# Kernel tuning notes

Measured on AMD Instinct MI355X. Metric: run time of the kernel, lower is better.

The kernel has to match this reference:

```python
import jax, jax.numpy as jnp
import numpy as np

D_MODEL = 1024
NHEADS = 16
DIM_K = D_MODEL // NHEADS


def setup_inputs() -> dict:
    key = jax.random.key(0)
    ks = jax.random.split(key, 7)
    B, S = 4, 2048
    scale = 1.0 / np.sqrt(D_MODEL)
    return {
        "Q": jax.random.normal(ks[0], (B, S, D_MODEL), jnp.float32),
        "K": jax.random.normal(ks[1], (B, S, D_MODEL), jnp.float32),
        "V": jax.random.normal(ks[2], (B, S, D_MODEL), jnp.float32),
        "Wq": jax.random.normal(ks[3], (D_MODEL, D_MODEL), jnp.float32) * scale,
        "Wk": jax.random.normal(ks[4], (D_MODEL, D_MODEL), jnp.float32) * scale,
        "Wv": jax.random.normal(ks[5], (D_MODEL, D_MODEL), jnp.float32) * scale,
        "Wo": jax.random.normal(ks[6], (D_MODEL, D_MODEL), jnp.float32) * scale,
    }


def _split(x):
    # [B,S,D] -> [B,H,S,dk]
    B, S, _ = x.shape
    return x.reshape(B, S, NHEADS, DIM_K).transpose(0, 2, 1, 3)


def reference(Q, K, V, Wq, Wk, Wv, Wo):
    # nn.Linear(x) = x @ W.T; weights stored torch-style [out, in]
    q = _split(Q @ Wq.T)  # [B,H,S,dk]
    k = _split(K @ Wk.T)
    v = _split(V @ Wv.T)
    scores = jnp.einsum("bhsd,bhtd->bhst", q, k) / jnp.sqrt(jnp.float32(DIM_K))
    attn = jax.nn.softmax(scores, axis=-1)
    out = jnp.einsum("bhst,bhtd->bhsd", attn, v)  # [B,H,S,dk]
    B, H, S, dk = out.shape
    out = out.transpose(0, 2, 1, 3).reshape(B, S, H * dk)
    return out @ Wo.T
```

## Files before the change

### kernel.cpp

```cpp
#include <hip/hip_runtime.h>
#include <math.h>
#include <stdint.h>

#define D_MODEL 1024
#define NHEADS  16
#define DK      64
#define BATCH   4
#define SEQ     2048
#define MROWS   (BATCH * SEQ)
#define TENS    ((size_t)MROWS * D_MODEL)
#define WELT    ((size_t)D_MODEL * D_MODEL)

typedef __attribute__((ext_vector_type(8))) _Float16 f16x8;
typedef __attribute__((ext_vector_type(2))) __fp16 h16x2;
typedef __attribute__((ext_vector_type(4))) float f32x4;
typedef __attribute__((ext_vector_type(8))) unsigned short us8;
typedef __attribute__((ext_vector_type(4))) unsigned short us4;

__device__ __forceinline__ unsigned short f2h(float x) {
    _Float16 h = (_Float16)x;
    return __builtin_bit_cast(unsigned short, h);
}

#if __has_builtin(__builtin_amdgcn_exp2f)
__device__ __forceinline__ float fexp2(float x) { return __builtin_amdgcn_exp2f(x); }
#else
__device__ __forceinline__ float fexp2(float x) { return exp2f(x); }
#endif

__device__ __forceinline__ void gld_lds16(const void* g, void* l) {
    __builtin_amdgcn_global_load_lds(
        (__attribute__((address_space(1))) void*)(uintptr_t)(g),
        (__attribute__((address_space(3))) void*)(unsigned)(uintptr_t)(l),
        16, 0, 0);
}

__global__ __launch_bounds__(256)
void convert_kernel(const float* __restrict__ q, const float* __restrict__ k,
                    const float* __restrict__ v, const float* __restrict__ wq,
                    const float* __restrict__ wk, const float* __restrict__ wv,
                    const float* __restrict__ wo, unsigned short* __restrict__ dst)
{
    const int seg = blockIdx.y;
    size_t i = ((size_t)blockIdx.x * 256 + threadIdx.x) * 4;
    const float* src;
    size_t doff, soff;
    if (seg < 3) {
        if (i >= TENS) return;
        src = (seg == 0) ? q : (seg == 1) ? k : v;
        soff = i;
        doff = (size_t)seg * TENS + i;
    } else {
        if (i >= 4 * WELT) return;
        const int widx = (int)(i >> 20);
        src = (widx == 0) ? wq : (widx == 1) ? wk : (widx == 2) ? wv : wo;
        soff = i & (WELT - 1);
        doff = 3 * TENS + i;
    }
    float4 f = *(const float4*)(src + soff);
    us4 o = { f2h(f.x), f2h(f.y), f2h(f.z), f2h(f.w) };
    *(us4*)(dst + doff) = o;
}

__device__ __forceinline__
void gemm_body8(const unsigned short* __restrict__ A,
                const unsigned short* __restrict__ B,
                void* __restrict__ C, int N, int K, int omode,
                int bm, int bn,
                unsigned short* As, unsigned short* Bs)
{
    const int tid  = threadIdx.x;
    const int wave = tid >> 6;
    const int lane = tid & 63;
    const int g    = lane >> 4;
    const int m15  = lane & 15;

    const int srw = lane >> 3;
    const int lc  = (lane & 7) ^ srw;

    const int wr = (wave >> 1) * 64;
    const int wc = (wave & 1) * 64;

    f32x4 acc[4][4];
#pragma unroll
    for (int i = 0; i < 4; ++i)
#pragma unroll
        for (int j = 0; j < 4; ++j) acc[i][j] = (f32x4){0.f, 0.f, 0.f, 0.f};

    auto stage = [&](int buf, int t) {
        const int k0 = t * 64;
#pragma unroll
        for (int i = 0; i < 4; ++i) {
            const int rb = i * 64 + wave * 8;
            gld_lds16(A + (size_t)(bm + rb + srw) * K + k0 + lc * 8,
                      &As[buf * (256 * 64) + rb * 64]);
        }
#pragma unroll
        for (int j = 0; j < 2; ++j) {
            const int rb = j * 64 + wave * 8;
            gld_lds16(B + (size_t)(bn + rb + srw) * K + k0 + lc * 8,
                      &Bs[buf * (128 * 64) + rb * 64]);
        }
    };

    auto compute = [&](int buf) {
        const unsigned short* Ab = &As[buf * (256 * 64)];
        const unsigned short* Bb = &Bs[buf * (128 * 64)];
#pragma unroll
        for (int t = 0; t < 2; ++t) {
            f16x8 af[4], bf[4];
#pragma unroll
            for (int i = 0; i < 4; ++i) {
                int row = wr + i * 16 + m15;
                int pc  = (4 * t + g) ^ (row & 7);
                af[i] = *(const f16x8*)&Ab[row * 64 + pc * 8];
            }
#pragma unroll
            for (int j = 0; j < 4; ++j) {
                int row = wc + j * 16 + m15;
                int pc  = (4 * t + g) ^ (row & 7);
                bf[j] = *(const f16x8*)&Bb[row * 64 + pc * 8];
            }
            __builtin_amdgcn_s_setprio(1);
#pragma unroll
            for (int i = 0; i < 4; ++i)
#pragma unroll
                for (int j = 0; j < 4; ++j)
                    acc[i][j] = __builtin_amdgcn_mfma_f32_16x16x32_f16(
                        af[i], bf[j], acc[i][j], 0, 0, 0);
            __builtin_amdgcn_s_setprio(0);
        }
    };

    const int NT = K / 64;
    stage(0, 0);
    stage(1, 1);
    int cur = 0;
    for (int t = 0; t < NT; ++t) {
        if (t + 2 < NT) {
            int nb = cur + 2; if (nb >= 3) nb -= 3;
            stage(nb, t + 2);
            asm volatile("s_waitcnt vmcnt(12)" ::: "memory");
        } else if (t + 1 < NT) {
            asm volatile("s_waitcnt vmcnt(6)" ::: "memory");
        } else {
            asm volatile("s_waitcnt vmcnt(0)" ::: "memory");
        }
        __builtin_amdgcn_s_barrier();
        __builtin_amdgcn_sched_barrier(0);
        compute(cur);
        __builtin_amdgcn_sched_barrier(0);
        __builtin_amdgcn_s_barrier();
        ++cur; if (cur == 3) cur = 0;
    }

#pragma unroll
    for (int i = 0; i < 4; ++i) {
        const int gm0 = bm + wr + i * 16 + g * 4;
#pragma unroll
        for (int j = 0; j < 4; ++j) {
            const int gn = bn + wc + j * 16 + m15;
            if (omode == 0) {
#pragma unroll
                for (int r = 0; r < 4; ++r)
                    ((float*)C)[(size_t)(gm0 + r) * N + gn] = acc[i][j][r];
            } else if (omode == 1) {
#pragma unroll
                for (int r = 0; r < 4; ++r)
                    ((unsigned short*)C)[(size_t)(gm0 + r) * N + gn] = f2h(acc[i][j][r]);
            } else {
                const int b_ = gm0 >> 11, s_ = gm0 & 2047;
                const int h_ = gn >> 6,  d_ = gn & 63;
                us4 o = { f2h(acc[i][j][0]), f2h(acc[i][j][1]),
                          f2h(acc[i][j][2]), f2h(acc[i][j][3]) };
                *(us4*)((unsigned short*)C +
                        (((size_t)(b_ * NHEADS + h_) * 256 + (s_ >> 3)) * 64 + d_) * 8
                        + (s_ & 7)) = o;
            }
        }
    }
}

__device__ __forceinline__ void panel_decode(int f, int& bm, int& bn) {
    const int x = f & 7;
    const int k = f >> 3;
    const int panel = x * 4 + (k >> 3);
    const int ny = k & 7;
    bm = panel * 256;
    bn = ny * 128;
}

__global__ __launch_bounds__(512)
void proj3_kernel(const unsigned short* __restrict__ qb,
                  const unsigned short* __restrict__ kb,
                  const unsigned short* __restrict__ vb,
                  const unsigned short* __restrict__ wq,
                  const unsigned short* __restrict__ wk,
                  const unsigned short* __restrict__ wv,
                  unsigned short* __restrict__ qproj,
                  unsigned short* __restrict__ kproj,
                  unsigned short* __restrict__ vtw)
{
    __shared__ unsigned short As[3 * 256 * 64];
    __shared__ unsigned short Bs[3 * 128 * 64];
    const int z = blockIdx.z;
    const unsigned short* A = (z == 0) ? qb : (z == 1) ? kb : vb;
    const unsigned short* B = (z == 0) ? wq : (z == 1) ? wk : wv;
    void* C = (z == 0) ? (void*)qproj : (z == 1) ? (void*)kproj : (void*)vtw;
    int bm, bn;
    panel_decode(blockIdx.x, bm, bn);
    gemm_body8(A, B, C, D_MODEL, D_MODEL, (z == 2) ? 2 : 1, bm, bn, As, Bs);
}

__global__ __launch_bounds__(512)
void gemm_out_kernel(const unsigned short* __restrict__ A,
                     const unsigned short* __restrict__ B,
                     float* __restrict__ C)
{
    __shared__ unsigned short As[3 * 256 * 64];
    __shared__ unsigned short Bs[3 * 128 * 64];
    int bm, bn;
    panel_decode(blockIdx.x, bm, bn);
    gemm_body8(A, B, C, D_MODEL, D_MODEL, 0, bm, bn, As, Bs);
}

__global__ __launch_bounds__(256, 2)
void attn_kernel(const unsigned short* __restrict__ qp,
                 const unsigned short* __restrict__ kp,
                 const unsigned short* __restrict__ vt,
                 unsigned short* __restrict__ ao)
{
    __shared__ unsigned short Ks[2][64 * 64];
    __shared__ unsigned short VTs[2][64 * 64];
    __shared__ unsigned short Ps[4][16 * 64];

    const int tid = threadIdx.x;
    const int w = tid >> 6, lane = tid & 63;
    const int g = lane >> 4, m15 = lane & 15;

    const int f = blockIdx.x;
    const int bh = (f & 7) * 8 + ((f >> 3) >> 3);
    const int qt = (f >> 3) & 7;
    const int b = bh >> 4, h = bh & 15;

    const int q0 = qt * 256 + w * 64;
    const size_t rowbase = (size_t)b * SEQ;

    const int srw = lane >> 3;
    const int lc  = (lane & 7) ^ srw;

    const _Float16 qscale = (_Float16)(0.125f * 1.4426950408889634f);
    f16x8 qf[4][2];
#pragma unroll
    for (int mi = 0; mi < 4; ++mi)
#pragma unroll
        for (int t = 0; t < 2; ++t) {
            f16x8 v = *(const f16x8*)(qp + (rowbase + q0 + mi * 16 + m15) * D_MODEL
                                      + h * DK + t * 32 + g * 8);
            qf[mi][t] = v * qscale;
        }

    const _Float16 one16 = (_Float16)1.f;
    const f16x8 onesf = { one16, one16, one16, one16, one16, one16, one16, one16 };

    float mrun[4] = {-INFINITY, -INFINITY, -INFINITY, -INFINITY};
    float lrun[4] = {0.f, 0.f, 0.f, 0.f};

    f32x4 accO[4][4];
#pragma unroll
    for (int mi = 0; mi < 4; ++mi)
#pragma unroll
        for (int i = 0; i < 4; ++i) accO[mi][i] = (f32x4){0.f, 0.f, 0.f, 0.f};

    const unsigned short* kbase = kp + rowbase * D_MODEL + h * DK;
    const unsigned short* vbase = vt + (size_t)(b * NHEADS + h) * DK * SEQ;

    auto stage = [&](int buf, int t) {
#pragma unroll
        for (int it = 0; it < 2; ++it) {
            const int rb = w * 16 + it * 8;
            gld_lds16(kbase + (size_t)(t * 64 + rb + srw) * D_MODEL + lc * 8,
                      &Ks[buf][rb * 64]);
            gld_lds16(vbase + ((size_t)(t * 8 + lc) * 64 + rb + srw) * 8,
                      &VTs[buf][rb * 64]);
        }
    };

    const int NT = SEQ / 64;
    stage(0, 0);
    __syncthreads();

    for (int kt = 0; kt < NT; ++kt) {
        const int cur = kt & 1;
        if (kt + 1 < NT) stage(cur ^ 1, kt + 1);

        f32x4 ST[4][4];
        __builtin_amdgcn_s_setprio(1);
#pragma unroll
        for (int km = 0; km < 4; ++km) {
            const int row = km * 16 + m15;
            f16x8 kf0 = *(const f16x8*)&Ks[cur][row * 64 + ((0 + g) ^ (row & 7)) * 8];
            f16x8 kf1 = *(const f16x8*)&Ks[cur][row * 64 + ((4 + g) ^ (row & 7)) * 8];
#pragma unroll
            for (int mi = 0; mi < 4; ++mi) {
                f32x4 z = (f32x4){0.f, 0.f, 0.f, 0.f};
                z = __builtin_amdgcn_mfma_f32_16x16x32_f16(kf0, qf[mi][0], z, 0, 0, 0);
                z = __builtin_amdgcn_mfma_f32_16x16x32_f16(kf1, qf[mi][1], z, 0, 0, 0);
                ST[km][mi] = z;
            }
        }
        __builtin_amdgcn_s_setprio(0);

        float lmx[4];
#pragma unroll
        for (int mi = 0; mi < 4; ++mi) {
            float t0 = fmaxf(fmaxf(ST[0][mi][0], ST[0][mi][1]), ST[0][mi][2]);
            float t1 = fmaxf(fmaxf(ST[0][mi][3], ST[1][mi][0]), ST[1][mi][1]);
            float t2 = fmaxf(fmaxf(ST[1][mi][2], ST[1][mi][3]), ST[2][mi][0]);
            float t3 = fmaxf(fmaxf(ST[2][mi][1], ST[2][mi][2]), ST[2][mi][3]);
            float t4 = fmaxf(fmaxf(ST[3][mi][0], ST[3][mi][1]), ST[3][mi][2]);
            float u0 = fmaxf(fmaxf(t0, t1), t2);
            float u1 = fmaxf(fmaxf(t3, t4), ST[3][mi][3]);
            lmx[mi] = fmaxf(u0, u1);
        }

        const float THR = 8.f;
        int need = (lmx[0] > mrun[0] + THR) | (lmx[1] > mrun[1] + THR) |
                   (lmx[2] > mrun[2] + THR) | (lmx[3] > mrun[3] + THR);
        if (__any(need)) {
#pragma unroll
            for (int mi = 0; mi < 4; ++mi) {
                float mx = fmaxf(lmx[mi], __shfl_xor(lmx[mi], 16));
                mx = fmaxf(mx, __shfl_xor(mx, 32));
                float mnew = fmaxf(mrun[mi], mx);
                float scl = fexp2(mrun[mi] - mnew);
                mrun[mi] = mnew;
                lrun[mi] *= scl;
#pragma unroll
                for (int i = 0; i < 4; ++i) accO[mi][i] *= scl;
            }
        }

        f16x8 pf[4][2];
#pragma unroll
        for (int mi = 0; mi < 4; ++mi) {
            const float mnew = mrun[mi];
#pragma unroll
            for (int km = 0; km < 4; ++km) {
                float p0 = fexp2(ST[km][mi][0] - mnew);
                float p1 = fexp2(ST[km][mi][1] - mnew);
                float p2 = fexp2(ST[km][mi][2] - mnew);
                float p3 = fexp2(ST[km][mi][3] - mnew);
                h16x2 d0 = __builtin_amdgcn_cvt_pkrtz(p0, p1);
                h16x2 d1 = __builtin_amdgcn_cvt_pkrtz(p2, p3);
                uint2 wv = { __builtin_bit_cast(unsigned, d0),
                             __builtin_bit_cast(unsigned, d1) };
                const int pc = (km * 2 + (g >> 1)) ^ (m15 & 7);
                *(uint2*)&Ps[w][m15 * 64 + pc * 8 + (g & 1) * 4] = wv;
            }
            pf[mi][0] = *(const f16x8*)&Ps[w][m15 * 64 + ((0 + g) ^ (m15 & 7)) * 8];
            pf[mi][1] = *(const f16x8*)&Ps[w][m15 * 64 + ((4 + g) ^ (m15 & 7)) * 8];
            f32x4 zs = (f32x4){0.f, 0.f, 0.f, 0.f};
            zs = __builtin_amdgcn_mfma_f32_16x16x32_f16(onesf, pf[mi][0], zs, 0, 0, 0);
            zs = __builtin_amdgcn_mfma_f32_16x16x32_f16(onesf, pf[mi][1], zs, 0, 0, 0);
            lrun[mi] += zs[0];
        }

        __builtin_amdgcn_s_setprio(1);
#pragma unroll
        for (int i = 0; i < 4; ++i) {
            const int row = i * 16 + m15;
            f16x8 vf0 = *(const f16x8*)&VTs[cur][row * 64 + ((0 + g) ^ (row & 7)) * 8];
            f16x8 vf1 = *(const f16x8*)&VTs[cur][row * 64 + ((4 + g) ^ (row & 7)) * 8];
#pragma unroll
            for (int mi = 0; mi < 4; ++mi) {
                f32x4 a = accO[mi][i];
                a = __builtin_amdgcn_mfma_f32_16x16x32_f16(vf0, pf[mi][0], a, 0, 0, 0);
                a = __builtin_amdgcn_mfma_f32_16x16x32_f16(vf1, pf[mi][1], a, 0, 0, 0);
                accO[mi][i] = a;
            }
        }
        __builtin_amdgcn_s_setprio(0);

        __syncthreads();
    }

#pragma unroll
    for (int mi = 0; mi < 4; ++mi) {
        const float li = 1.f / lrun[mi];
        const size_t qg = rowbase + q0 + mi * 16 + m15;
#pragma unroll
        for (int i = 0; i < 4; ++i) {
            us4 o = { f2h(accO[mi][i][0] * li), f2h(accO[mi][i][1] * li),
                      f2h(accO[mi][i][2] * li), f2h(accO[mi][i][3] * li) };
            *(us4*)(ao + qg * D_MODEL + h * DK + i * 16 + g * 4) = o;
        }
    }
}

extern "C" void kernel_launch(void* const* d_in, const int* in_sizes, int n_in,
                              void* d_out, int out_size, void* d_ws, size_t ws_size,
                              hipStream_t stream)
{
    const float* Q  = (const float*)d_in[0];
    const float* K  = (const float*)d_in[1];
    const float* V  = (const float*)d_in[2];
    const float* Wq = (const float*)d_in[3];
    const float* Wk = (const float*)d_in[4];
    const float* Wv = (const float*)d_in[5];
    const float* Wo = (const float*)d_in[6];

    unsigned short* base = (unsigned short*)d_ws;
    unsigned short* qb = base;
    unsigned short* kb = qb + TENS;
    unsigned short* vb = kb + TENS;
    unsigned short* wq = vb + TENS;
    unsigned short* wk = wq + WELT;
    unsigned short* wv = wk + WELT;
    unsigned short* wo = wv + WELT;
    unsigned short* qproj = wo + WELT;
    unsigned short* kproj = qproj + TENS;
    unsigned short* vtw   = kproj + TENS;
    unsigned short* aow   = vtw + TENS;

    convert_kernel<<<dim3(TENS / 1024, 4), 256, 0, stream>>>(Q, K, V, Wq, Wk, Wv, Wo, base);

    proj3_kernel<<<dim3(256, 1, 3), 512, 0, stream>>>(
        qb, kb, vb, wq, wk, wv, qproj, kproj, vtw);

    attn_kernel<<<dim3(512, 1, 1), 256, 0, stream>>>(
        qproj, kproj, vtw, aow);

    gemm_out_kernel<<<dim3(256, 1, 1), 512, 0, stream>>>(
        aow, wo, (float*)d_out);
}
```

Measured before the change: 320.6 us.

## Fuse fp32-to-fp16 activation conversion into projection GEMM loads

The separate convert pass over Q, K and V is removed. The projection GEMM now loads fp32 activations into registers, converts them to fp16 and writes them to LDS itself, using a new double-buffered pipeline with two blocks per CU. This drops a full read/write round trip of three 32 MB tensors plus their fp16 copies. In exchange the GEMM reads twice as many bytes for A and carries more register pressure. Separately, the attention kernel now writes all four P tiles to shared memory before reading any back, which enlarges Ps to 32 KB.

```diff
diff --git a/kernel.cpp b/kernel.cpp
--- a/kernel.cpp
+++ b/kernel.cpp
@@ -36,36 +36,194 @@
 }
 
 __global__ __launch_bounds__(256)
-void convert_kernel(const float* __restrict__ q, const float* __restrict__ k,
-                    const float* __restrict__ v, const float* __restrict__ wq,
-                    const float* __restrict__ wk, const float* __restrict__ wv,
-                    const float* __restrict__ wo, unsigned short* __restrict__ dst)
-{
-    const int seg = blockIdx.y;
+void convert_w_kernel(const float* __restrict__ wq, const float* __restrict__ wk,
+                      const float* __restrict__ wv, const float* __restrict__ wo,
+                      unsigned short* __restrict__ dst)
+{
     size_t i = ((size_t)blockIdx.x * 256 + threadIdx.x) * 4;
-    const float* src;
-    size_t doff, soff;
-    if (seg < 3) {
-        if (i >= TENS) return;
-        src = (seg == 0) ? q : (seg == 1) ? k : v;
-        soff = i;
-        doff = (size_t)seg * TENS + i;
-    } else {
-        if (i >= 4 * WELT) return;
-        const int widx = (int)(i >> 20);
-        src = (widx == 0) ? wq : (widx == 1) ? wk : (widx == 2) ? wv : wo;
-        soff = i & (WELT - 1);
-        doff = 3 * TENS + i;
-    }
+    const int widx = (int)(i >> 20);
+    const float* src = (widx == 0) ? wq : (widx == 1) ? wk : (widx == 2) ? wv : wo;
+    const size_t soff = i & (WELT - 1);
     float4 f = *(const float4*)(src + soff);
     us4 o = { f2h(f.x), f2h(f.y), f2h(f.z), f2h(f.w) };
-    *(us4*)(dst + doff) = o;
+    *(us4*)(dst + i) = o;
+}
+
+__device__ __forceinline__ void panel_decode(int f, int& bm, int& bn) {
+    const int x = f & 7;
+    const int k = f >> 3;
+    const int panel = x * 4 + (k >> 3);
+    const int ny = k & 7;
+    bm = panel * 256;
+    bn = ny * 128;
+}
+
+__device__ __forceinline__
+void gemm_body_cvt(const float* __restrict__ A32,
+                   const unsigned short* __restrict__ Bh,
+                   void* __restrict__ C, int N, int K, int omode,
+                   int bm, int bn,
+                   unsigned short* As, unsigned short* Bs)
+{
+    const int tid  = threadIdx.x;
+    const int wave = tid >> 6;
+    const int lane = tid & 63;
+    const int g    = lane >> 4;
+    const int m15  = lane & 15;
+
+    const int srw = lane >> 3;
+    const int lc  = (lane & 7) ^ srw;
+
+    const int wr = (wave >> 1) * 64;
+    const int wc = (wave & 1) * 64;
+
+    const int arow = tid >> 1;
+    const int ac0  = (tid & 1) * 4;
+
+    f32x4 acc[4][4];
+#pragma unroll
+    for (int i = 0; i < 4; ++i)
+#pragma unroll
+        for (int j = 0; j < 4; ++j) acc[i][j] = (f32x4){0.f, 0.f, 0.f, 0.f};
+
+    auto loadA = [&](float4* r, int t) {
+        const float* s = A32 + (size_t)(bm + arow) * K + t * 64 + ac0 * 8;
+#pragma unroll
+        for (int c = 0; c < 4; ++c) {
+            r[2 * c]     = *(const float4*)(s + c * 8);
+            r[2 * c + 1] = *(const float4*)(s + c * 8 + 4);
+        }
+    };
+    auto writeA = [&](int buf, const float4* r) {
+#pragma unroll
+        for (int c = 0; c < 4; ++c) {
+            us8 o = { f2h(r[2*c].x),   f2h(r[2*c].y),   f2h(r[2*c].z),   f2h(r[2*c].w),
+                      f2h(r[2*c+1].x), f2h(r[2*c+1].y), f2h(r[2*c+1].z), f2h(r[2*c+1].w) };
+            const int pc = (ac0 + c) ^ (arow & 7);
+            *(us8*)&As[buf * (256 * 64) + arow * 64 + pc * 8] = o;
+        }
+    };
+    auto gldB = [&](int buf, int t) {
+        const int k0 = t * 64;
+#pragma unroll
+        for (int j = 0; j < 2; ++j) {
+            const int rb = j * 64 + wave * 8;
+            gld_lds16(Bh + (size_t)(bn + rb + srw) * K + k0 + lc * 8,
+                      &Bs[buf * (128 * 64) + rb * 64]);
+        }
+    };
+    auto compute = [&](int buf) {
+        const unsigned short* Ab = &As[buf * (256 * 64)];
+        const unsigned short* Bb = &Bs[buf * (128 * 64)];
+#pragma unroll
+        for (int t = 0; t < 2; ++t) {
+            f16x8 af[4], bf[4];
+#pragma unroll
+            for (int i = 0; i < 4; ++i) {
+                int row = wr + i * 16 + m15;
+                int pc  = (4 * t + g) ^ (row & 7);
+                af[i] = *(const f16x8*)&Ab[row * 64 + pc * 8];
+            }
+#pragma unroll
+            for (int j = 0; j < 4; ++j) {
+                int row = wc + j * 16 + m15;
+                int pc  = (4 * t + g) ^ (row & 7);
+                bf[j] = *(const f16x8*)&Bb[row * 64 + pc * 8];
+            }
+            __builtin_amdgcn_s_setprio(1);
+#pragma unroll
+            for (int i = 0; i < 4; ++i)
+#pragma unroll
+                for (int j = 0; j < 4; ++j)
+                    acc[i][j] = __builtin_amdgcn_mfma_f32_16x16x32_f16(
+                        af[i], bf[j], acc[i][j], 0, 0, 0);
+            __builtin_amdgcn_s_setprio(0);
+        }
+    };
+
+    const int NT = K / 64;
+    float4 rA0[8], rA1[8];
+    loadA(rA0, 0);
+    gldB(0, 0);
+    loadA(rA1, 1);
+    asm volatile("s_waitcnt vmcnt(10)" ::: "memory");
+    writeA(0, rA0);
+    asm volatile("s_waitcnt vmcnt(8)" ::: "memory");
+    asm volatile("s_waitcnt lgkmcnt(0)" ::: "memory");
+    __builtin_amdgcn_s_barrier();
+    gldB(1, 1);
+
+#pragma unroll
+    for (int t = 0; t < NT; ++t) {
+        const int cb = t & 1;
+        float4* rnext = (t & 1) ? rA1 : rA0;
+        float4* rpend = (t & 1) ? rA0 : rA1;
+        if (t + 2 < NT) loadA(rnext, t + 2);
+        if (t + 1 < NT) {
+            if (t + 2 < NT) { asm volatile("s_waitcnt vmcnt(10)" ::: "memory"); }
+            else            { asm volatile("s_waitcnt vmcnt(2)" ::: "memory"); }
+            writeA(cb ^ 1, rpend);
+        }
+        __builtin_amdgcn_sched_barrier(0);
+        compute(cb);
+        __builtin_amdgcn_sched_barrier(0);
+        if (t + 1 < NT) {
+            if (t + 2 < NT) { asm volatile("s_waitcnt vmcnt(8)" ::: "memory"); }
+            else            { asm volatile("s_waitcnt vmcnt(0)" ::: "memory"); }
+            asm volatile("s_waitcnt lgkmcnt(0)" ::: "memory");
+            __builtin_amdgcn_s_barrier();
+            if (t + 2 < NT) gldB(cb, t + 2);
+        }
+    }
+
+#pragma unroll
+    for (int i = 0; i < 4; ++i) {
+        const int gm0 = bm + wr + i * 16 + g * 4;
+#pragma unroll
+        for (int j = 0; j < 4; ++j) {
+            const int gn = bn + wc + j * 16 + m15;
+            if (omode == 1) {
+#pragma unroll
+                for (int r = 0; r < 4; ++r)
+                    ((unsigned short*)C)[(size_t)(gm0 + r) * N + gn] = f2h(acc[i][j][r]);
+            } else {
+                const int b_ = gm0 >> 11, s_ = gm0 & 2047;
+                const int h_ = gn >> 6,  d_ = gn & 63;
+                us4 o = { f2h(acc[i][j][0]), f2h(acc[i][j][1]),
+                          f2h(acc[i][j][2]), f2h(acc[i][j][3]) };
+                *(us4*)((unsigned short*)C +
+                        (((size_t)(b_ * NHEADS + h_) * 256 + (s_ >> 3)) * 64 + d_) * 8
+                        + (s_ & 7)) = o;
+            }
+        }
+    }
+}
+
+__global__ __launch_bounds__(512, 2)
+void proj3_kernel(const float* __restrict__ Q, const float* __restrict__ K,
+                  const float* __restrict__ V,
+                  const unsigned short* __restrict__ wq,
+                  const unsigned short* __restrict__ wk,
+                  const unsigned short* __restrict__ wv,
+                  unsigned short* __restrict__ qproj,
+                  unsigned short* __restrict__ kproj,
+                  unsigned short* __restrict__ vtw)
+{
+    __shared__ unsigned short As[2 * 256 * 64];
+    __shared__ unsigned short Bs[2 * 128 * 64];
+    const int z = blockIdx.z;
+    const float* A = (z == 0) ? Q : (z == 1) ? K : V;
+    const unsigned short* B = (z == 0) ? wq : (z == 1) ? wk : wv;
+    void* C = (z == 0) ? (void*)qproj : (z == 1) ? (void*)kproj : (void*)vtw;
+    int bm, bn;
+    panel_decode(blockIdx.x, bm, bn);
+    gemm_body_cvt(A, B, C, D_MODEL, D_MODEL, (z == 2) ? 2 : 1, bm, bn, As, Bs);
 }
 
 __device__ __forceinline__
 void gemm_body8(const unsigned short* __restrict__ A,
                 const unsigned short* __restrict__ B,
-                void* __restrict__ C, int N, int K, int omode,
+                float* __restrict__ C, int N, int K,
                 int bm, int bn,
                 unsigned short* As, unsigned short* Bs)
 {
@@ -160,56 +318,11 @@
 #pragma unroll
         for (int j = 0; j < 4; ++j) {
             const int gn = bn + wc + j * 16 + m15;
-            if (omode == 0) {
-#pragma unroll
-                for (int r = 0; r < 4; ++r)
-                    ((float*)C)[(size_t)(gm0 + r) * N + gn] = acc[i][j][r];
-            } else if (omode == 1) {
-#pragma unroll
-                for (int r = 0; r < 4; ++r)
-                    ((unsigned short*)C)[(size_t)(gm0 + r) * N + gn] = f2h(acc[i][j][r]);
-            } else {
-                const int b_ = gm0 >> 11, s_ = gm0 & 2047;
-                const int h_ = gn >> 6,  d_ = gn & 63;
-                us4 o = { f2h(acc[i][j][0]), f2h(acc[i][j][1]),
-                          f2h(acc[i][j][2]), f2h(acc[i][j][3]) };
-                *(us4*)((unsigned short*)C +
-                        (((size_t)(b_ * NHEADS + h_) * 256 + (s_ >> 3)) * 64 + d_) * 8
-                        + (s_ & 7)) = o;
-            }
+#pragma unroll
+            for (int r = 0; r < 4; ++r)
+                C[(size_t)(gm0 + r) * N + gn] = acc[i][j][r];
         }
     }
-}
-
-__device__ __forceinline__ void panel_decode(int f, int& bm, int& bn) {
-    const int x = f & 7;
-    const int k = f >> 3;
-    const int panel = x * 4 + (k >> 3);
-    const int ny = k & 7;
-    bm = panel * 256;
-    bn = ny * 128;
-}
-
-__global__ __launch_bounds__(512)
-void proj3_kernel(const unsigned short* __restrict__ qb,
-                  const unsigned short* __restrict__ kb,
-                  const unsigned short* __restrict__ vb,
-                  const unsigned short* __restrict__ wq,
-                  const unsigned short* __restrict__ wk,
-                  const unsigned short* __restrict__ wv,
-                  unsigned short* __restrict__ qproj,
-                  unsigned short* __restrict__ kproj,
-                  unsigned short* __restrict__ vtw)
-{
-    __shared__ unsigned short As[3 * 256 * 64];
-    __shared__ unsigned short Bs[3 * 128 * 64];
-    const int z = blockIdx.z;
-    const unsigned short* A = (z == 0) ? qb : (z == 1) ? kb : vb;
-    const unsigned short* B = (z == 0) ? wq : (z == 1) ? wk : wv;
-    void* C = (z == 0) ? (void*)qproj : (z == 1) ? (void*)kproj : (void*)vtw;
-    int bm, bn;
-    panel_decode(blockIdx.x, bm, bn);
-    gemm_body8(A, B, C, D_MODEL, D_MODEL, (z == 2) ? 2 : 1, bm, bn, As, Bs);
 }
 
 __global__ __launch_bounds__(512)
@@ -221,7 +334,7 @@
     __shared__ unsigned short Bs[3 * 128 * 64];
     int bm, bn;
     panel_decode(blockIdx.x, bm, bn);
-    gemm_body8(A, B, C, D_MODEL, D_MODEL, 0, bm, bn, As, Bs);
+    gemm_body8(A, B, C, D_MODEL, D_MODEL, bm, bn, As, Bs);
 }
 
 __global__ __launch_bounds__(256, 2)
@@ -232,7 +345,7 @@
 {
     __shared__ unsigned short Ks[2][64 * 64];
     __shared__ unsigned short VTs[2][64 * 64];
-    __shared__ unsigned short Ps[4][16 * 64];
+    __shared__ unsigned short Ps[4][64 * 64];
 
     const int tid = threadIdx.x;
     const int w = tid >> 6, lane = tid & 63;
@@ -341,10 +454,10 @@
             }
         }
 
-        f16x8 pf[4][2];
 #pragma unroll
         for (int mi = 0; mi < 4; ++mi) {
             const float mnew = mrun[mi];
+            const int prow = mi * 16 + m15;
 #pragma unroll
             for (int km = 0; km < 4; ++km) {
                 float p0 = fexp2(ST[km][mi][0] - mnew);
@@ -356,10 +469,18 @@
                 uint2 wv = { __builtin_bit_cast(unsigned, d0),
                              __builtin_bit_cast(unsigned, d1) };
                 const int pc = (km * 2 + (g >> 1)) ^ (m15 & 7);
-                *(uint2*)&Ps[w][m15 * 64 + pc * 8 + (g & 1) * 4] = wv;
-            }
-            pf[mi][0] = *(const f16x8*)&Ps[w][m15 * 64 + ((0 + g) ^ (m15 & 7)) * 8];
-            pf[mi][1] = *(const f16x8*)&Ps[w][m15 * 64 + ((4 + g) ^ (m15 & 7)) * 8];
+                *(uint2*)&Ps[w][prow * 64 + pc * 8 + (g & 1) * 4] = wv;
+            }
+        }
+        f16x8 pf[4][2];
+#pragma unroll
+        for (int mi = 0; mi < 4; ++mi) {
+            const int prow = mi * 16 + m15;
+            pf[mi][0] = *(const f16x8*)&Ps[w][prow * 64 + ((0 + g) ^ (m15 & 7)) * 8];
+            pf[mi][1] = *(const f16x8*)&Ps[w][prow * 64 + ((4 + g) ^ (m15 & 7)) * 8];
+        }
+#pragma unroll
+        for (int mi = 0; mi < 4; ++mi) {
             f32x4 zs = (f32x4){0.f, 0.f, 0.f, 0.f};
             zs = __builtin_amdgcn_mfma_f32_16x16x32_f16(onesf, pf[mi][0], zs, 0, 0, 0);
             zs = __builtin_amdgcn_mfma_f32_16x16x32_f16(onesf, pf[mi][1], zs, 0, 0, 0);
@@ -411,10 +532,7 @@
     const float* Wo = (const float*)d_in[6];
 
     unsigned short* base = (unsigned short*)d_ws;
-    unsigned short* qb = base;
-    unsigned short* kb = qb + TENS;
-    unsigned short* vb = kb + TENS;
-    unsigned short* wq = vb + TENS;
+    unsigned short* wq = base;
     unsigned short* wk = wq + WELT;
     unsigned short* wv = wk + WELT;
     unsigned short* wo = wv + WELT;
@@ -423,10 +541,10 @@
     unsigned short* vtw   = kproj + TENS;
     unsigned short* aow   = vtw + TENS;
 
-    convert_kernel<<<dim3(TENS / 1024, 4), 256, 0, stream>>>(Q, K, V, Wq, Wk, Wv, Wo, base);
+    convert_w_kernel<<<dim3(4 * WELT / 1024), 256, 0, stream>>>(Wq, Wk, Wv, Wo, wq);
 
     proj3_kernel<<<dim3(256, 1, 3), 512, 0, stream>>>(
-        qb, kb, vb, wq, wk, wv, qproj, kproj, vtw);
+        Q, K, V, wq, wk, wv, qproj, kproj, vtw);
 
     attn_kernel<<<dim3(512, 1, 1), 256, 0, stream>>>(
         qproj, kproj, vtw, aow);
```

Measured after the change: 399.0 us. 1.24x slower.
